# Performance work log

Hardware: AMD Instinct MI355X
Metric: run time of the kernel (lower is better)

## Reference

```python
import jax, jax.numpy as jnp
import numpy as np


def setup_inputs() -> dict:
    key = jax.random.key(0)
    ks = jax.random.split(key, 7)
    B, T, I, H, O = 256, 512, 64, 512, 24
    s_ih = 1.0 / np.sqrt(H)
    return {
        "x":    jax.random.normal(ks[0], (B, T, I), dtype=jnp.float32),
        "W_ih": jax.random.normal(ks[1], (H, I), dtype=jnp.float32) * s_ih,
        "W_hh": jax.random.normal(ks[2], (H, H), dtype=jnp.float32) * s_ih,
        "b_ih": jax.random.normal(ks[3], (H,), dtype=jnp.float32) * s_ih,
        "b_hh": jax.random.normal(ks[4], (H,), dtype=jnp.float32) * s_ih,
        "fc_w": jax.random.normal(ks[5], (O, H), dtype=jnp.float32) * s_ih,
        "fc_b": jax.random.normal(ks[6], (O,), dtype=jnp.float32) * s_ih,
    }


def reference(x, W_ih, W_hh, b_ih, b_hh, fc_w, fc_b):
    # PyTorch nn.RNN(nonlinearity='relu', batch_first=True):
    #   h_t = relu(x_t @ W_ih^T + b_ih + h_{t-1} @ W_hh^T + b_hh), h_0 = 0
    B, T, I = x.shape
    H = W_hh.shape[0]
    # Precompute input projections for all timesteps in one GEMM: [B, T, H]
    xw = jnp.einsum('bti,hi->bth', x, W_ih) + (b_ih + b_hh)

    def step(h, xw_t):
        h = jax.nn.relu(xw_t + h @ W_hh.T)  # [B, H]
        return h, None

    h0 = jnp.zeros((B, H), dtype=x.dtype)
    h_last, _ = jax.lax.scan(step, h0, jnp.swapaxes(xw, 0, 1))  # scan over T
    # Final linear on last timestep's hidden state: [B, O]
    return h_last @ fc_w.T + fc_b
```

## Files before the change

### kernel.cpp

```cpp
#include <hip/hip_runtime.h>


#define T_STEPS 512
#define NG      16
#define NM      8
#define SLAB    32768
#define FLAGS_OFF (2 * NG * SLAB)
#define POLL_CAP 100000
#define TAG_CAP  20000

#define LA_STRIDE 1040
#define LA_PLANE  16640
#define LA_PAR    33280
#define LX_OFF    66560
#define LX_STRIDE 144
#define LX_PLANE  2304

typedef short          short8  __attribute__((ext_vector_type(8)));
typedef unsigned short bfx4    __attribute__((ext_vector_type(4)));
typedef unsigned       uintx4  __attribute__((ext_vector_type(4)));
typedef float          floatx4 __attribute__((ext_vector_type(4)));
typedef unsigned long long ull;

__device__ __forceinline__ unsigned short f2bf(float x) {
    unsigned u = __float_as_uint(x);
    u = (u + 0x7fffu + ((u >> 16) & 1u)) >> 16;
    return (unsigned short)u;
}
__device__ __forceinline__ float bf2f(unsigned short h) {
    return __uint_as_float(((unsigned)h) << 16);
}
__device__ __forceinline__ unsigned cvtpk(float a, float b) {
    unsigned r;
    asm("v_cvt_pk_bf16_f32 %0, %1, %2" : "=v"(r) : "v"(a), "v"(b));
    return r;
}
__device__ __forceinline__ void pack_hilo(float f0, float f1, float f2, float f3,
                                          ull& hi, ull& lo) {
    const unsigned h01 = cvtpk(f0, f1), h23 = cvtpk(f2, f3);
    const float l0 = f0 - __uint_as_float(h01 << 16);
    const float l1 = f1 - __uint_as_float(h01 & 0xffff0000u);
    const float l2 = f2 - __uint_as_float(h23 << 16);
    const float l3 = f3 - __uint_as_float(h23 & 0xffff0000u);
    const unsigned q01 = cvtpk(l0, l1), q23 = cvtpk(l2, l3);
    hi = (ull)h01 | ((ull)h23 << 32);
    lo = (ull)q01 | ((ull)q23 << 32);
}
__device__ __forceinline__ void st_ag_u32(void* p, unsigned v) {
    __hip_atomic_store((unsigned*)p, v, __ATOMIC_RELAXED, __HIP_MEMORY_SCOPE_AGENT);
}
__device__ __forceinline__ unsigned ld_ag_u32(const void* p) {
    return __hip_atomic_load((const unsigned*)p, __ATOMIC_RELAXED, __HIP_MEMORY_SCOPE_AGENT);
}
__device__ __forceinline__ uintx4 ld_l3_b128_async(const void* p) {
    uintx4 v;
    asm volatile("global_load_dwordx4 %0, %1, off sc0 sc1"
                 : "=v"(v) : "v"(p) : "memory");
    return v;
}
__device__ __forceinline__ void st_l3_b32(void* p, unsigned v) {
    asm volatile("global_store_dword %0, %1, off sc0 sc1"
                 :: "v"(p), "v"(v) : "memory");
}
__device__ __forceinline__ void st_l3_b128(void* p, uintx4 v) {
    asm volatile("global_store_dwordx4 %0, %1, off sc0 sc1"
                 :: "v"(p), "v"(v) : "memory");
}
__device__ __forceinline__ void wait_vm0() {
    asm volatile("s_waitcnt vmcnt(0)" ::: "memory");
}
__device__ __forceinline__ void poll_flag(const unsigned* p, unsigned want) {
    int it = 0;
    for (;;) {
        unsigned f = ld_ag_u32(p);
        if (f == want || f == want + 1u) return;
        if (++it >= POLL_CAP) return;
    }
}

__global__ __launch_bounds__(256, 1) void rnn_persistent(
    const float* __restrict__ x,     const float* __restrict__ W_ih,
    const float* __restrict__ W_hh,  const float* __restrict__ b_ih,
    const float* __restrict__ b_hh,  const float* __restrict__ fc_w,
    const float* __restrict__ fc_b,  float* __restrict__ out,
    unsigned char* __restrict__ ws)
{
    const int tid  = threadIdx.x;
    const int lane = tid & 63;
    const int w    = tid >> 6;
    const int n    = lane & 15;
    const int quad = lane >> 4;

    const int bid = blockIdx.x;
    const int g = bid >> 3;
    const int m = bid & 7;

    unsigned char* ex = (unsigned char*)ws;
    unsigned* flagbase = (unsigned*)(ex + FLAGS_OFF + g * 64);
    __shared__ __align__(16) unsigned char smem[LX_OFF + 2 * LX_PLANE];

    const int wrow = m * 64 + w * 16 + n;
    short8 Whi[18], Wlo[18];
    #pragma unroll
    for (int kt = 0; kt < 18; ++kt) {
        const float* p = (kt < 16) ? (W_hh + wrow * 512 + kt * 32 + quad * 8)
                                   : (W_ih + wrow * 64 + (kt - 16) * 32 + quad * 8);
        #pragma unroll
        for (int jj = 0; jj < 8; ++jj) {
            float f = p[jj];
            unsigned short h = f2bf(f);
            Whi[kt][jj] = (short)h;
            Wlo[kt][jj] = (short)f2bf(f - bf2f(h));
        }
    }
    const float bias_i = b_ih[wrow] + b_hh[wrow];

    const int prow = tid >> 4, pc4 = tid & 15;
    int poff[7];
    #pragma unroll
    for (int r = 0; r < 7; ++r) {
        const int pm = r + (r >= m ? 1 : 0);
        poff[r] = prow * 2048 + pm * 256 + pc4 * 16;
    }

    {
        uintx4 z = {0u, 0u, 0u, 0u};
        st_l3_b128(ex + g * SLAB + prow * 2048 + m * 256 + pc4 * 16, z);
        #pragma unroll
        for (int r = 0; r < 4; ++r) {
            const int row = quad * 4 + r;
            *(unsigned short*)(smem + 0 * LA_PLANE + row * LA_STRIDE + wrow * 2) = 0;
            *(unsigned short*)(smem + LA_PLANE + row * LA_STRIDE + wrow * 2) = 0;
        }
    }
    wait_vm0();
    __syncthreads();
    if (tid == 0) st_ag_u32(flagbase + m, 1u);

    const int xrow = tid >> 4, xi4 = tid & 15;
    const float* xbase = x + (size_t)(g * 16 + xrow) * T_STEPS * 64 + xi4 * 4;
    float4 xv_cur = *(const float4*)(xbase + 0 * 64);
    for (int t = 0; t < T_STEPS; ++t) {
        const unsigned texp = (((unsigned)t >> 1) & 1u) << 31;
        const unsigned char* slab_r = ex + ((t & 1) * NG + g) * SLAB;

        uintx4 P[7];
        #pragma unroll
        for (int r = 0; r < 7; ++r) P[r] = ld_l3_b128_async(slab_r + poff[r]);

        if (tid < 7) {
            const int pm = tid + (tid >= m ? 1 : 0);
            poll_flag(flagbase + pm, (unsigned)t + 1u);
        }
        wait_vm0();
        __syncthreads();

        {
            int it = 0;
            for (;;) {
                unsigned bad = 0;
                #pragma unroll
                for (int r = 0; r < 7; ++r)
                    bad |= (P[r].x ^ texp) | (P[r].y ^ texp)
                         | (P[r].z ^ texp) | (P[r].w ^ texp);
                if (!(bad & 0x80000000u) || ++it >= TAG_CAP) break;
                #pragma unroll
                for (int r = 0; r < 7; ++r) P[r] = ld_l3_b128_async(slab_r + poff[r]);
                wait_vm0();
            }
        }

        const int tn = (t + 1 < T_STEPS) ? (t + 1) : (T_STEPS - 1);
        const float4 xv_nxt = *(const float4*)(xbase + (size_t)tn * 64);

        unsigned char* abase = smem + (t & 1) * LA_PAR;
        #pragma unroll
        for (int r = 0; r < 7; ++r) {
            const int pm = r + (r >= m ? 1 : 0);
            ull hi, lo;
            pack_hilo(__uint_as_float(P[r].x & 0x7fffffffu),
                      __uint_as_float(P[r].y & 0x7fffffffu),
                      __uint_as_float(P[r].z & 0x7fffffffu),
                      __uint_as_float(P[r].w & 0x7fffffffu), hi, lo);
            const int base = prow * LA_STRIDE + pm * 128 + pc4 * 8;
            *(ull*)(abase + base)            = hi;
            *(ull*)(abase + LA_PLANE + base) = lo;
        }
        {
            ull hi, lo;
            pack_hilo(xv_cur.x, xv_cur.y, xv_cur.z, xv_cur.w, hi, lo);
            *(ull*)(smem + LX_OFF + xrow * LX_STRIDE + xi4 * 8)            = hi;
            *(ull*)(smem + LX_OFF + LX_PLANE + xrow * LX_STRIDE + xi4 * 8) = lo;
        }
        __syncthreads();

        floatx4 c0 = {0.f,0.f,0.f,0.f}, c1 = {0.f,0.f,0.f,0.f}, c2 = {0.f,0.f,0.f,0.f};
        #pragma unroll
        for (int kt = 0; kt < 16; ++kt) {
            const unsigned char* ba = abase + n * LA_STRIDE + kt * 64 + quad * 16;
            short8 ah = *(const short8*)(ba);
            short8 al = *(const short8*)(ba + LA_PLANE);
            c0 = __builtin_amdgcn_mfma_f32_16x16x32_bf16(ah, Whi[kt], c0, 0, 0, 0);
            c1 = __builtin_amdgcn_mfma_f32_16x16x32_bf16(al, Whi[kt], c1, 0, 0, 0);
            c2 = __builtin_amdgcn_mfma_f32_16x16x32_bf16(ah, Wlo[kt], c2, 0, 0, 0);
        }
        #pragma unroll
        for (int kt = 16; kt < 18; ++kt) {
            const unsigned char* ba = smem + LX_OFF + n * LX_STRIDE + (kt - 16) * 64 + quad * 16;
            short8 ah = *(const short8*)(ba);
            short8 al = *(const short8*)(ba + LX_PLANE);
            c0 = __builtin_amdgcn_mfma_f32_16x16x32_bf16(ah, Whi[kt], c0, 0, 0, 0);
            c1 = __builtin_amdgcn_mfma_f32_16x16x32_bf16(al, Whi[kt], c1, 0, 0, 0);
            c2 = __builtin_amdgcn_mfma_f32_16x16x32_bf16(ah, Wlo[kt], c2, 0, 0, 0);
        }

        const unsigned otag = ((((unsigned)t + 1u) >> 1) & 1u) << 31;
        unsigned char* slab_w = ex + (((t + 1) & 1) * NG + g) * SLAB;
        unsigned char* obase  = smem + ((t + 1) & 1) * LA_PAR;
        const floatx4 cs = c0 + c1 + c2;
        const int r0 = quad * 4;
        {
            const float v0 = fmaxf(cs[0] + bias_i, 0.f);
            const float v1 = fmaxf(cs[1] + bias_i, 0.f);
            const float v2 = fmaxf(cs[2] + bias_i, 0.f);
            const float v3 = fmaxf(cs[3] + bias_i, 0.f);
            st_l3_b32(slab_w + (r0+0) * 2048 + wrow * 4, __float_as_uint(v0) | otag);
            st_l3_b32(slab_w + (r0+1) * 2048 + wrow * 4, __float_as_uint(v1) | otag);
            st_l3_b32(slab_w + (r0+2) * 2048 + wrow * 4, __float_as_uint(v2) | otag);
            st_l3_b32(slab_w + (r0+3) * 2048 + wrow * 4, __float_as_uint(v3) | otag);
            const unsigned h01 = cvtpk(v0, v1), h23 = cvtpk(v2, v3);
            const float l0 = v0 - __uint_as_float(h01 << 16);
            const float l1 = v1 - __uint_as_float(h01 & 0xffff0000u);
            const float l2 = v2 - __uint_as_float(h23 << 16);
            const float l3 = v3 - __uint_as_float(h23 & 0xffff0000u);
            const unsigned q01 = cvtpk(l0, l1), q23 = cvtpk(l2, l3);
            *(unsigned short*)(obase + (r0+0) * LA_STRIDE + wrow * 2) = (unsigned short)(h01 & 0xffffu);
            *(unsigned short*)(obase + (r0+1) * LA_STRIDE + wrow * 2) = (unsigned short)(h01 >> 16);
            *(unsigned short*)(obase + (r0+2) * LA_STRIDE + wrow * 2) = (unsigned short)(h23 & 0xffffu);
            *(unsigned short*)(obase + (r0+3) * LA_STRIDE + wrow * 2) = (unsigned short)(h23 >> 16);
            *(unsigned short*)(obase + LA_PLANE + (r0+0) * LA_STRIDE + wrow * 2) = (unsigned short)(q01 & 0xffffu);
            *(unsigned short*)(obase + LA_PLANE + (r0+1) * LA_STRIDE + wrow * 2) = (unsigned short)(q01 >> 16);
            *(unsigned short*)(obase + LA_PLANE + (r0+2) * LA_STRIDE + wrow * 2) = (unsigned short)(q23 & 0xffffu);
            *(unsigned short*)(obase + LA_PLANE + (r0+3) * LA_STRIDE + wrow * 2) = (unsigned short)(q23 >> 16);
        }
        if (tid == 0) st_ag_u32(flagbase + m, (unsigned)t + 2u);
        xv_cur = xv_nxt;
    }

    if (m != 0) return;
    {
        const unsigned texp = 0;
        const unsigned char* slab_r = ex + (0 * NG + g) * SLAB;
        uintx4 P[7];
        #pragma unroll
        for (int r = 0; r < 7; ++r) P[r] = ld_l3_b128_async(slab_r + poff[r]);
        if (tid < 7) poll_flag(flagbase + (tid + 1), (unsigned)T_STEPS + 1u);
        wait_vm0();
        __syncthreads();
        int it = 0;
        for (;;) {
            unsigned bad = 0;
            #pragma unroll
            for (int r = 0; r < 7; ++r)
                bad |= (P[r].x ^ texp) | (P[r].y ^ texp)
                     | (P[r].z ^ texp) | (P[r].w ^ texp);
            if (!(bad & 0x80000000u) || ++it >= TAG_CAP) break;
            #pragma unroll
            for (int r = 0; r < 7; ++r) P[r] = ld_l3_b128_async(slab_r + poff[r]);
            wait_vm0();
        }
        unsigned char* abase = smem;
        #pragma unroll
        for (int r = 0; r < 7; ++r) {
            const int pm = r + 1;
            ull hi, lo;
            pack_hilo(__uint_as_float(P[r].x & 0x7fffffffu),
                      __uint_as_float(P[r].y & 0x7fffffffu),
                      __uint_as_float(P[r].z & 0x7fffffffu),
                      __uint_as_float(P[r].w & 0x7fffffffu), hi, lo);
            const int base = prow * LA_STRIDE + pm * 128 + pc4 * 8;
            *(ull*)(abase + base)            = hi;
            *(ull*)(abase + LA_PLANE + base) = lo;
        }
    }
    __syncthreads();
    for (int idx = tid; idx < 384; idx += 256) {
        const int row = idx / 24, o = idx % 24;
        const float* wp = fc_w + o * 512;
        float s = 0.f;
        for (int k = 0; k < 512; k += 4) {
            bfx4 hv = *(const bfx4*)(smem + row * LA_STRIDE + k * 2);
            bfx4 lv = *(const bfx4*)(smem + LA_PLANE + row * LA_STRIDE + k * 2);
            const float4 wv = *(const float4*)(wp + k);
            s += (bf2f(hv[0]) + bf2f(lv[0])) * wv.x;
            s += (bf2f(hv[1]) + bf2f(lv[1])) * wv.y;
            s += (bf2f(hv[2]) + bf2f(lv[2])) * wv.z;
            s += (bf2f(hv[3]) + bf2f(lv[3])) * wv.w;
        }
        out[(g * 16 + row) * 24 + o] = s + fc_b[o];
    }
}

extern "C" void kernel_launch(void* const* d_in, const int* in_sizes, int n_in,
                              void* d_out, int out_size, void* d_ws, size_t ws_size,
                              hipStream_t stream) {
    (void)in_sizes; (void)n_in; (void)out_size; (void)ws_size;
    const float* x    = (const float*)d_in[0];
    const float* W_ih = (const float*)d_in[1];
    const float* W_hh = (const float*)d_in[2];
    const float* b_ih = (const float*)d_in[3];
    const float* b_hh = (const float*)d_in[4];
    const float* fc_w = (const float*)d_in[5];
    const float* fc_b = (const float*)d_in[6];
    rnn_persistent<<<NG * NM, 256, 0, stream>>>(x, W_ih, W_hh, b_ih, b_hh,
                                                fc_w, fc_b, (float*)d_out,
                                                (unsigned char*)d_ws);
}
```

Before: 1.456 ms.

## Split K across two wave groups per block with LDS reduction

Doubles the block size to 512 threads, so each column group of 4 waves is duplicated and the 18 K-tiles of the recurrent MFMA chain are split 9/9 between two halves. Partial accumulators are reduced through a new LDS region. The peer-slab loads are spread across all 512 threads, and each block's flag moves to its own 64-byte slot. The intent is to shorten the serial per-step MFMA dependency chain and halve weight registers per thread, at the cost of an extra __syncthreads and an LDS round trip each timestep.

```diff
diff --git a/kernel.cpp b/kernel.cpp
--- a/kernel.cpp
+++ b/kernel.cpp
@@ -15,6 +15,8 @@
 #define LX_OFF    66560
 #define LX_STRIDE 144
 #define LX_PLANE  2304
+#define LRED_OFF  71168
+#define LDS_TOT   75264
 
 typedef short          short8  __attribute__((ext_vector_type(8)));
 typedef unsigned short bfx4    __attribute__((ext_vector_type(4)));
@@ -77,8 +79,13 @@
         if (++it >= POLL_CAP) return;
     }
 }
-
-__global__ __launch_bounds__(256, 1) void rnn_persistent(
+__device__ __forceinline__ unsigned* flag_ptr(unsigned char* ex, int g, int mm) {
+    return (unsigned*)(ex + FLAGS_OFF) + ((g * NM + mm) << 4);
+}
+
+#define MFMA_BF16 __builtin_amdgcn_mfma_f32_16x16x32_bf16
+
+__global__ __launch_bounds__(512, 2) void rnn_persistent(
     const float* __restrict__ x,     const float* __restrict__ W_ih,
     const float* __restrict__ W_hh,  const float* __restrict__ b_ih,
     const float* __restrict__ b_hh,  const float* __restrict__ fc_w,
@@ -90,67 +97,80 @@
     const int w    = tid >> 6;
     const int n    = lane & 15;
     const int quad = lane >> 4;
+    const int cw   = w & 3;
+    const int kh   = w >> 2;
 
     const int bid = blockIdx.x;
     const int g = bid >> 3;
     const int m = bid & 7;
 
     unsigned char* ex = (unsigned char*)ws;
-    unsigned* flagbase = (unsigned*)(ex + FLAGS_OFF + g * 64);
-    __shared__ __align__(16) unsigned char smem[LX_OFF + 2 * LX_PLANE];
-
-    const int wrow = m * 64 + w * 16 + n;
-    short8 Whi[18], Wlo[18];
+    __shared__ __align__(16) unsigned char smem[LDS_TOT];
+
+    const int wrow = m * 64 + cw * 16 + n;
+    short8 Whi[9], Wlo[9];
     #pragma unroll
-    for (int kt = 0; kt < 18; ++kt) {
+    for (int j = 0; j < 9; ++j) {
+        const int kt = kh * 9 + j;
         const float* p = (kt < 16) ? (W_hh + wrow * 512 + kt * 32 + quad * 8)
                                    : (W_ih + wrow * 64 + (kt - 16) * 32 + quad * 8);
         #pragma unroll
         for (int jj = 0; jj < 8; ++jj) {
             float f = p[jj];
             unsigned short h = f2bf(f);
-            Whi[kt][jj] = (short)h;
-            Wlo[kt][jj] = (short)f2bf(f - bf2f(h));
+            Whi[j][jj] = (short)h;
+            Wlo[j][jj] = (short)f2bf(f - bf2f(h));
         }
     }
     const float bias_i = b_ih[wrow] + b_hh[wrow];
 
-    const int prow = tid >> 4, pc4 = tid & 15;
-    int poff[7];
+    const int tau = (tid + 256) & 511;
+    const int NU  = (tau < 256) ? 4 : 3;
+    int uoff[4], lbs[4];
     #pragma unroll
-    for (int r = 0; r < 7; ++r) {
-        const int pm = r + (r >= m ? 1 : 0);
-        poff[r] = prow * 2048 + pm * 256 + pc4 * 16;
-    }
-
-    {
+    for (int k = 0; k < 4; ++k) {
+        const int u = tau + 512 * k;
+        if (u < 1792) {
+            const int p  = u >> 8;
+            const int pm = p + (p >= m ? 1 : 0);
+            const int rw = (u >> 4) & 15;
+            const int pc = u & 15;
+            uoff[k] = rw * 2048 + pm * 256 + pc * 16;
+            lbs[k]  = rw * LA_STRIDE + pm * 128 + pc * 8;
+        } else { uoff[k] = 0; lbs[k] = 0; }
+    }
+
+    if (tid < 256) {
+        const int pr = tid >> 4, pc = tid & 15;
         uintx4 z = {0u, 0u, 0u, 0u};
-        st_l3_b128(ex + g * SLAB + prow * 2048 + m * 256 + pc4 * 16, z);
-        #pragma unroll
-        for (int r = 0; r < 4; ++r) {
-            const int row = quad * 4 + r;
-            *(unsigned short*)(smem + 0 * LA_PLANE + row * LA_STRIDE + wrow * 2) = 0;
-            *(unsigned short*)(smem + LA_PLANE + row * LA_STRIDE + wrow * 2) = 0;
-        }
+        st_l3_b128(ex + g * SLAB + pr * 2048 + m * 256 + pc * 16, z);
+    }
+    #pragma unroll
+    for (int r = 0; r < 4; ++r) {
+        const int row = quad * 4 + r;
+        *(unsigned short*)(smem + row * LA_STRIDE + wrow * 2) = 0;
+        *(unsigned short*)(smem + LA_PLANE + row * LA_STRIDE + wrow * 2) = 0;
     }
     wait_vm0();
     __syncthreads();
-    if (tid == 0) st_ag_u32(flagbase + m, 1u);
+    if (tid == 0) st_ag_u32(flag_ptr(ex, g, m), 1u);
 
     const int xrow = tid >> 4, xi4 = tid & 15;
-    const float* xbase = x + (size_t)(g * 16 + xrow) * T_STEPS * 64 + xi4 * 4;
-    float4 xv_cur = *(const float4*)(xbase + 0 * 64);
+    const float* xbase = x + (size_t)(g * 16 + (xrow & 15)) * T_STEPS * 64 + xi4 * 4;
+    float4 xv_cur = {0.f, 0.f, 0.f, 0.f};
+    if (tid < 256) xv_cur = *(const float4*)(xbase);
     for (int t = 0; t < T_STEPS; ++t) {
         const unsigned texp = (((unsigned)t >> 1) & 1u) << 31;
         const unsigned char* slab_r = ex + ((t & 1) * NG + g) * SLAB;
 
-        uintx4 P[7];
+        uintx4 P[4];
         #pragma unroll
-        for (int r = 0; r < 7; ++r) P[r] = ld_l3_b128_async(slab_r + poff[r]);
+        for (int k = 0; k < 4; ++k) if (k < NU)
+            P[k] = ld_l3_b128_async(slab_r + uoff[k]);
 
         if (tid < 7) {
             const int pm = tid + (tid >= m ? 1 : 0);
-            poll_flag(flagbase + pm, (unsigned)t + 1u);
+            poll_flag(flag_ptr(ex, g, pm), (unsigned)t + 1u);
         }
         wait_vm0();
         __syncthreads();
@@ -160,33 +180,35 @@
             for (;;) {
                 unsigned bad = 0;
                 #pragma unroll
-                for (int r = 0; r < 7; ++r)
-                    bad |= (P[r].x ^ texp) | (P[r].y ^ texp)
-                         | (P[r].z ^ texp) | (P[r].w ^ texp);
+                for (int k = 0; k < 4; ++k) if (k < NU)
+                    bad |= (P[k].x ^ texp) | (P[k].y ^ texp)
+                         | (P[k].z ^ texp) | (P[k].w ^ texp);
                 if (!(bad & 0x80000000u) || ++it >= TAG_CAP) break;
                 #pragma unroll
-                for (int r = 0; r < 7; ++r) P[r] = ld_l3_b128_async(slab_r + poff[r]);
+                for (int k = 0; k < 4; ++k) if (k < NU)
+                    P[k] = ld_l3_b128_async(slab_r + uoff[k]);
                 wait_vm0();
             }
         }
 
-        const int tn = (t + 1 < T_STEPS) ? (t + 1) : (T_STEPS - 1);
-        const float4 xv_nxt = *(const float4*)(xbase + (size_t)tn * 64);
+        float4 xv_nxt = xv_cur;
+        if (tid < 256) {
+            const int tn = (t + 1 < T_STEPS) ? (t + 1) : (T_STEPS - 1);
+            xv_nxt = *(const float4*)(xbase + (size_t)tn * 64);
+        }
 
         unsigned char* abase = smem + (t & 1) * LA_PAR;
         #pragma unroll
-        for (int r = 0; r < 7; ++r) {
-            const int pm = r + (r >= m ? 1 : 0);
+        for (int k = 0; k < 4; ++k) if (k < NU) {
             ull hi, lo;
-            pack_hilo(__uint_as_float(P[r].x & 0x7fffffffu),
-                      __uint_as_float(P[r].y & 0x7fffffffu),
-                      __uint_as_float(P[r].z & 0x7fffffffu),
-                      __uint_as_float(P[r].w & 0x7fffffffu), hi, lo);
-            const int base = prow * LA_STRIDE + pm * 128 + pc4 * 8;
-            *(ull*)(abase + base)            = hi;
-            *(ull*)(abase + LA_PLANE + base) = lo;
-        }
-        {
+            pack_hilo(__uint_as_float(P[k].x & 0x7fffffffu),
+                      __uint_as_float(P[k].y & 0x7fffffffu),
+                      __uint_as_float(P[k].z & 0x7fffffffu),
+                      __uint_as_float(P[k].w & 0x7fffffffu), hi, lo);
+            *(ull*)(abase + lbs[k])            = hi;
+            *(ull*)(abase + LA_PLANE + lbs[k]) = lo;
+        }
+        if (tid < 256) {
             ull hi, lo;
             pack_hilo(xv_cur.x, xv_cur.y, xv_cur.z, xv_cur.w, hi, lo);
             *(ull*)(smem + LX_OFF + xrow * LX_STRIDE + xi4 * 8)            = hi;
@@ -195,31 +217,47 @@
         __syncthreads();
 
         floatx4 c0 = {0.f,0.f,0.f,0.f}, c1 = {0.f,0.f,0.f,0.f}, c2 = {0.f,0.f,0.f,0.f};
-        #pragma unroll
-        for (int kt = 0; kt < 16; ++kt) {
-            const unsigned char* ba = abase + n * LA_STRIDE + kt * 64 + quad * 16;
-            short8 ah = *(const short8*)(ba);
-            short8 al = *(const short8*)(ba + LA_PLANE);
-            c0 = __builtin_amdgcn_mfma_f32_16x16x32_bf16(ah, Whi[kt], c0, 0, 0, 0);
-            c1 = __builtin_amdgcn_mfma_f32_16x16x32_bf16(al, Whi[kt], c1, 0, 0, 0);
-            c2 = __builtin_amdgcn_mfma_f32_16x16x32_bf16(ah, Wlo[kt], c2, 0, 0, 0);
-        }
-        #pragma unroll
-        for (int kt = 16; kt < 18; ++kt) {
-            const unsigned char* ba = smem + LX_OFF + n * LX_STRIDE + (kt - 16) * 64 + quad * 16;
-            short8 ah = *(const short8*)(ba);
-            short8 al = *(const short8*)(ba + LX_PLANE);
-            c0 = __builtin_amdgcn_mfma_f32_16x16x32_bf16(ah, Whi[kt], c0, 0, 0, 0);
-            c1 = __builtin_amdgcn_mfma_f32_16x16x32_bf16(al, Whi[kt], c1, 0, 0, 0);
-            c2 = __builtin_amdgcn_mfma_f32_16x16x32_bf16(ah, Wlo[kt], c2, 0, 0, 0);
-        }
-
-        const unsigned otag = ((((unsigned)t + 1u) >> 1) & 1u) << 31;
-        unsigned char* slab_w = ex + (((t + 1) & 1) * NG + g) * SLAB;
-        unsigned char* obase  = smem + ((t + 1) & 1) * LA_PAR;
-        const floatx4 cs = c0 + c1 + c2;
-        const int r0 = quad * 4;
-        {
+        if (kh == 0) {
+            #pragma unroll
+            for (int j = 0; j < 9; ++j) {
+                const unsigned char* ba = abase + n * LA_STRIDE + j * 64 + quad * 16;
+                short8 ah = *(const short8*)(ba);
+                short8 al = *(const short8*)(ba + LA_PLANE);
+                c0 = MFMA_BF16(ah, Whi[j], c0, 0, 0, 0);
+                c1 = MFMA_BF16(al, Whi[j], c1, 0, 0, 0);
+                c2 = MFMA_BF16(ah, Wlo[j], c2, 0, 0, 0);
+            }
+        } else {
+            #pragma unroll
+            for (int j = 0; j < 7; ++j) {
+                const unsigned char* ba = abase + n * LA_STRIDE + (9 + j) * 64 + quad * 16;
+                short8 ah = *(const short8*)(ba);
+                short8 al = *(const short8*)(ba + LA_PLANE);
+                c0 = MFMA_BF16(ah, Whi[j], c0, 0, 0, 0);
+                c1 = MFMA_BF16(al, Whi[j], c1, 0, 0, 0);
+                c2 = MFMA_BF16(ah, Wlo[j], c2, 0, 0, 0);
+            }
+            #pragma unroll
+            for (int j = 7; j < 9; ++j) {
+                const unsigned char* ba = smem + LX_OFF + n * LX_STRIDE + (j - 7) * 64 + quad * 16;
+                short8 ah = *(const short8*)(ba);
+                short8 al = *(const short8*)(ba + LX_PLANE);
+                c0 = MFMA_BF16(ah, Whi[j], c0, 0, 0, 0);
+                c1 = MFMA_BF16(al, Whi[j], c1, 0, 0, 0);
+                c2 = MFMA_BF16(ah, Wlo[j], c2, 0, 0, 0);
+            }
+        }
+
+        floatx4 cs = c0 + c1 + c2;
+        unsigned char* redp = smem + LRED_OFF + ((cw * 64 + lane) << 4);
+        if (kh == 1) *(floatx4*)redp = cs;
+        __syncthreads();
+        if (kh == 0) {
+            cs += *(const floatx4*)redp;
+            const unsigned otag = ((((unsigned)t + 1u) >> 1) & 1u) << 31;
+            unsigned char* slab_w = ex + (((t + 1) & 1) * NG + g) * SLAB;
+            unsigned char* obase  = smem + ((t + 1) & 1) * LA_PAR;
+            const int r0 = quad * 4;
             const float v0 = fmaxf(cs[0] + bias_i, 0.f);
             const float v1 = fmaxf(cs[1] + bias_i, 0.f);
             const float v2 = fmaxf(cs[2] + bias_i, 0.f);
@@ -243,7 +281,7 @@
             *(unsigned short*)(obase + LA_PLANE + (r0+2) * LA_STRIDE + wrow * 2) = (unsigned short)(q23 & 0xffffu);
             *(unsigned short*)(obase + LA_PLANE + (r0+3) * LA_STRIDE + wrow * 2) = (unsigned short)(q23 >> 16);
         }
-        if (tid == 0) st_ag_u32(flagbase + m, (unsigned)t + 2u);
+        if (tid == 0) st_ag_u32(flag_ptr(ex, g, m), (unsigned)t + 2u);
         xv_cur = xv_nxt;
     }
 
@@ -251,53 +289,61 @@
     {
         const unsigned texp = 0;
         const unsigned char* slab_r = ex + (0 * NG + g) * SLAB;
-        uintx4 P[7];
-        #pragma unroll
-        for (int r = 0; r < 7; ++r) P[r] = ld_l3_b128_async(slab_r + poff[r]);
-        if (tid < 7) poll_flag(flagbase + (tid + 1), (unsigned)T_STEPS + 1u);
+        uintx4 P7[7]; int po[7];
+        if (tid < 256) {
+            const int pr = tid >> 4, pc = tid & 15;
+            #pragma unroll
+            for (int r = 0; r < 7; ++r) {
+                po[r] = pr * 2048 + (r + 1) * 256 + pc * 16;
+                P7[r] = ld_l3_b128_async(slab_r + po[r]);
+            }
+        }
+        if (tid < 7) poll_flag(flag_ptr(ex, g, tid + 1), (unsigned)T_STEPS + 1u);
         wait_vm0();
         __syncthreads();
-        int it = 0;
-        for (;;) {
-            unsigned bad = 0;
-            #pragma unroll
-            for (int r = 0; r < 7; ++r)
-                bad |= (P[r].x ^ texp) | (P[r].y ^ texp)
-                     | (P[r].z ^ texp) | (P[r].w ^ texp);
-            if (!(bad & 0x80000000u) || ++it >= TAG_CAP) break;
-            #pragma unroll
-            for (int r = 0; r < 7; ++r) P[r] = ld_l3_b128_async(slab_r + poff[r]);
-            wait_vm0();
-        }
-        unsigned char* abase = smem;
-        #pragma unroll
-        for (int r = 0; r < 7; ++r) {
-            const int pm = r + 1;
-            ull hi, lo;
-            pack_hilo(__uint_as_float(P[r].x & 0x7fffffffu),
-                      __uint_as_float(P[r].y & 0x7fffffffu),
-                      __uint_as_float(P[r].z & 0x7fffffffu),
-                      __uint_as_float(P[r].w & 0x7fffffffu), hi, lo);
-            const int base = prow * LA_STRIDE + pm * 128 + pc4 * 8;
-            *(ull*)(abase + base)            = hi;
-            *(ull*)(abase + LA_PLANE + base) = lo;
-        }
-    }
-    __syncthreads();
-    for (int idx = tid; idx < 384; idx += 256) {
-        const int row = idx / 24, o = idx % 24;
-        const float* wp = fc_w + o * 512;
-        float s = 0.f;
-        for (int k = 0; k < 512; k += 4) {
-            bfx4 hv = *(const bfx4*)(smem + row * LA_STRIDE + k * 2);
-            bfx4 lv = *(const bfx4*)(smem + LA_PLANE + row * LA_STRIDE + k * 2);
-            const float4 wv = *(const float4*)(wp + k);
-            s += (bf2f(hv[0]) + bf2f(lv[0])) * wv.x;
-            s += (bf2f(hv[1]) + bf2f(lv[1])) * wv.y;
-            s += (bf2f(hv[2]) + bf2f(lv[2])) * wv.z;
-            s += (bf2f(hv[3]) + bf2f(lv[3])) * wv.w;
-        }
-        out[(g * 16 + row) * 24 + o] = s + fc_b[o];
+        if (tid < 256) {
+            const int pr = tid >> 4, pc = tid & 15;
+            int it = 0;
+            for (;;) {
+                unsigned bad = 0;
+                #pragma unroll
+                for (int r = 0; r < 7; ++r)
+                    bad |= (P7[r].x ^ texp) | (P7[r].y ^ texp)
+                         | (P7[r].z ^ texp) | (P7[r].w ^ texp);
+                if (!(bad & 0x80000000u) || ++it >= TAG_CAP) break;
+                #pragma unroll
+                for (int r = 0; r < 7; ++r) P7[r] = ld_l3_b128_async(slab_r + po[r]);
+                wait_vm0();
+            }
+            #pragma unroll
+            for (int r = 0; r < 7; ++r) {
+                const int pm = r + 1;
+                ull hi, lo;
+                pack_hilo(__uint_as_float(P7[r].x & 0x7fffffffu),
+                          __uint_as_float(P7[r].y & 0x7fffffffu),
+                          __uint_as_float(P7[r].z & 0x7fffffffu),
+                          __uint_as_float(P7[r].w & 0x7fffffffu), hi, lo);
+                const int base = pr * LA_STRIDE + pm * 128 + pc * 8;
+                *(ull*)(smem + base)            = hi;
+                *(ull*)(smem + LA_PLANE + base) = lo;
+            }
+        }
+        __syncthreads();
+        for (int idx = tid; idx < 384; idx += 512) {
+            const int row = idx / 24, o = idx % 24;
+            const float* wp = fc_w + o * 512;
+            float s = 0.f;
+            for (int k = 0; k < 512; k += 4) {
+                bfx4 hv = *(const bfx4*)(smem + row * LA_STRIDE + k * 2);
+                bfx4 lv = *(const bfx4*)(smem + LA_PLANE + row * LA_STRIDE + k * 2);
+                const float4 wv = *(const float4*)(wp + k);
+                s += (bf2f(hv[0]) + bf2f(lv[0])) * wv.x;
+                s += (bf2f(hv[1]) + bf2f(lv[1])) * wv.y;
+                s += (bf2f(hv[2]) + bf2f(lv[2])) * wv.z;
+                s += (bf2f(hv[3]) + bf2f(lv[3])) * wv.w;
+            }
+            out[(g * 16 + row) * 24 + o] = s + fc_b[o];
+        }
     }
 }
 
@@ -312,7 +358,7 @@
     const float* b_hh = (const float*)d_in[4];
     const float* fc_w = (const float*)d_in[5];
     const float* fc_b = (const float*)d_in[6];
-    rnn_persistent<<<NG * NM, 256, 0, stream>>>(x, W_ih, W_hh, b_ih, b_hh,
+    rnn_persistent<<<NG * NM, 512, 0, stream>>>(x, W_ih, W_hh, b_ih, b_hh,
                                                 fc_w, fc_b, (float*)d_out,
                                                 (unsigned char*)d_ws);
 }
```

Result: slower. 1.537 ms (+5.6%).
